# Performance work log

Measured on AMD Instinct MI355X. Metric: run time of the kernel, lower is better.

Reference implementation:

```python
import jax, jax.numpy as jnp
import numpy as np

B, IN_DIM, D, P = 256, 1024, 512, 2048


def setup_inputs() -> dict:
    key = jax.random.key(0)
    ks = jax.random.split(key, 7)
    return {
        "x": jax.random.normal(ks[0], (B, IN_DIM), dtype=jnp.float32),
        "y": jax.random.randint(ks[1], (B,), 0, P),
        "Wb": jax.random.normal(ks[2], (D, IN_DIM), dtype=jnp.float32) * 0.02,
        "bb": jax.random.normal(ks[3], (D,), dtype=jnp.float32) * 0.02,
        "Wm": jax.random.normal(ks[4], (P, D), dtype=jnp.float32) * 0.02,
        "bm": jax.random.normal(ks[5], (P,), dtype=jnp.float32) * 0.02,
        "proxies": jax.random.normal(ks[6], (P, D), dtype=jnp.float32),
    }


def reference(x, y, Wb, bb, Wm, bm, proxies):
    # backbone: Linear(in_dim -> D)
    feat = x @ Wb.T + bb                         # [B, D]
    # L2-norm regularizer: mean of per-row L2 norms
    reg_e = jnp.mean(jnp.sqrt(jnp.sum(feat * feat, axis=1)))
    # multi: classification head Linear(D -> P)
    out = feat @ Wm.T + bm                       # [B, P]
    # squared euclidean distance to each proxy (broadcast diff + square + sum)
    den = jnp.sum((feat[:, None, :] - proxies[None, :, :]) ** 2, axis=2)  # [B, P]
    # cross-entropy on negated distances
    logp = jax.nn.log_softmax(-den, axis=1)      # [B, P]
    loss = -jnp.mean(jnp.take_along_axis(logp, y[:, None], axis=1))
    return out, loss, reg_e
```

## Files before the change

kernel.cpp:

```cpp
#include <hip/hip_runtime.h>
#include <hip/hip_bf16.h>
#include <math.h>

#define NB   256
#define KIN  1024
#define ND   512
#define NP   2048
#define NTOT 4096

typedef __bf16 bf16x8 __attribute__((ext_vector_type(8)));
typedef float  f32x4  __attribute__((ext_vector_type(4)));
typedef unsigned short ush8 __attribute__((ext_vector_type(8)));

#define OFF_WPB    0u
#define OFF_FEAT32 4194304u
#define OFF_FEATB  4718592u
#define OFF_PN2    4980736u
#define OFF_LOGITS 4988928u

__device__ __forceinline__ ush8 pack8(float4 f0, float4 f1) {
    union { ush8 v; __hip_bfloat162 h[4]; } o;
    o.h[0] = __float22bfloat162_rn(make_float2(f0.x, f0.y));
    o.h[1] = __float22bfloat162_rn(make_float2(f0.z, f0.w));
    o.h[2] = __float22bfloat162_rn(make_float2(f1.x, f1.y));
    o.h[3] = __float22bfloat162_rn(make_float2(f1.z, f1.w));
    return o.v;
}
__device__ __forceinline__ unsigned short f2bf(float v) {
    union { __hip_bfloat16 h; unsigned short u; } c;
    c.h = __float2bfloat16(v);
    return c.u;
}

__global__ __launch_bounds__(256) void k_fa(
    const float* __restrict__ x, const float* __restrict__ Wb,
    const float* __restrict__ bb,
    const float* __restrict__ Wm, const float* __restrict__ prox,
    unsigned short* __restrict__ WPb, float* __restrict__ pn2,
    float* __restrict__ feat32, unsigned short* __restrict__ featb,
    float* __restrict__ tail)
{
    __shared__ unsigned short As[2][64 * 32];
    __shared__ unsigned short Bs[2][64 * 32];
    const int t = threadIdx.x, lane = t & 63, w = t >> 6;

    if (blockIdx.x >= 32) {
        const int pb = blockIdx.x - 32;
        if (pb == 0 && t < 2) tail[t] = 0.f;
#pragma unroll
        for (int i = 0; i < 4; ++i) {
            const int r = pb * 16 + w * 4 + i;
            const float* src = (r < NP) ? (Wm + (size_t)r * ND)
                                        : (prox + (size_t)(r - NP) * ND);
            float4 v0 = *(const float4*)(src + lane * 8);
            float4 v1 = *(const float4*)(src + lane * 8 + 4);
            if (r < NP) {
                *(ush8*)(WPb + (size_t)r * ND + lane * 8) = pack8(v0, v1);
            } else {
                float s = v0.x*v0.x + v0.y*v0.y + v0.z*v0.z + v0.w*v0.w
                        + v1.x*v1.x + v1.y*v1.y + v1.z*v1.z + v1.w*v1.w;
#pragma unroll
                for (int off = 32; off; off >>= 1) s += __shfl_down(s, off);
                if (lane == 0) pn2[r - NP] = s;
                float4 d0 = make_float4(v0.x + v0.x, v0.y + v0.y,
                                        v0.z + v0.z, v0.w + v0.w);
                float4 d1 = make_float4(v1.x + v1.x, v1.y + v1.y,
                                        v1.z + v1.z, v1.w + v1.w);
                *(ush8*)(WPb + (size_t)r * ND + lane * 8) = pack8(d0, d1);
            }
        }
        return;
    }

    const int m0 = (blockIdx.x >> 3) * 64, n0 = (blockIdx.x & 7) * 64;
    const int srow = t >> 2, sc = (t & 3) * 8;
    const float* gA = x  + (size_t)(m0 + srow) * KIN + sc;
    const float* gB = Wb + (size_t)(n0 + srow) * KIN + sc;
    float4 a0 = *(const float4*)gA, a1 = *(const float4*)(gA + 4);
    float4 b0 = *(const float4*)gB, b1 = *(const float4*)(gB + 4);
    f32x4 acc[2][2] = {};
    const int wm = (w >> 1) * 32, wn = (w & 1) * 32;
    const int fr = lane & 15, fcol = (lane >> 4) * 8;

    for (int ks = 0; ks < KIN / 32; ++ks) {
        *(ush8*)&As[ks & 1][srow * 32 + sc] = pack8(a0, a1);
        *(ush8*)&Bs[ks & 1][srow * 32 + sc] = pack8(b0, b1);
        __syncthreads();
        if (ks + 1 < KIN / 32) {
            a0 = *(const float4*)(gA + (ks + 1) * 32);
            a1 = *(const float4*)(gA + (ks + 1) * 32 + 4);
            b0 = *(const float4*)(gB + (ks + 1) * 32);
            b1 = *(const float4*)(gB + (ks + 1) * 32 + 4);
        }
        const unsigned short* as = &As[ks & 1][0];
        const unsigned short* bs = &Bs[ks & 1][0];
        bf16x8 af0 = *(const bf16x8*)&as[(wm      + fr) * 32 + fcol];
        bf16x8 af1 = *(const bf16x8*)&as[(wm + 16 + fr) * 32 + fcol];
        bf16x8 bf0 = *(const bf16x8*)&bs[(wn      + fr) * 32 + fcol];
        bf16x8 bf1 = *(const bf16x8*)&bs[(wn + 16 + fr) * 32 + fcol];
        acc[0][0] = __builtin_amdgcn_mfma_f32_16x16x32_bf16(af0, bf0, acc[0][0], 0, 0, 0);
        acc[0][1] = __builtin_amdgcn_mfma_f32_16x16x32_bf16(af0, bf1, acc[0][1], 0, 0, 0);
        acc[1][0] = __builtin_amdgcn_mfma_f32_16x16x32_bf16(af1, bf0, acc[1][0], 0, 0, 0);
        acc[1][1] = __builtin_amdgcn_mfma_f32_16x16x32_bf16(af1, bf1, acc[1][1], 0, 0, 0);
    }

    const int q = lane >> 4;
#pragma unroll
    for (int i = 0; i < 2; ++i)
#pragma unroll
        for (int j = 0; j < 2; ++j) {
            const int n = n0 + wn + 16 * j + fr;
            const float bbn = bb[n];
#pragma unroll
            for (int r = 0; r < 4; ++r) {
                const int m = m0 + wm + 16 * i + q * 4 + r;
                const float v = acc[i][j][r] + bbn;
                feat32[m * ND + n] = v;
                featb [m * ND + n] = f2bf(v);
            }
        }
}

__global__ __launch_bounds__(256) void k_fb(
    const unsigned short* __restrict__ featb,
    const unsigned short* __restrict__ WPb,
    const float* __restrict__ bm, const float* __restrict__ pn2,
    float* __restrict__ out, float* __restrict__ logits)
{
    __shared__ unsigned short As[2][64 * 32];
    __shared__ unsigned short Bs[2][64 * 32];
    const int t = threadIdx.x, lane = t & 63, w = t >> 6;
    const int n0 = blockIdx.x * 64;
    const int m0 = blockIdx.y * 64;
    const int srow = t >> 2, sc = (t & 3) * 8;
    const unsigned short* gA = featb + (size_t)(m0 + srow) * ND + sc;
    const unsigned short* gB = WPb   + (size_t)(n0 + srow) * ND + sc;
    ush8 va = *(const ush8*)gA;
    ush8 vb = *(const ush8*)gB;
    f32x4 acc[2][2] = {};
    const int wm = (w >> 1) * 32, wn = (w & 1) * 32;
    const int fr = lane & 15, fcol = (lane >> 4) * 8;

    for (int ks = 0; ks < ND / 32; ++ks) {
        *(ush8*)&As[ks & 1][srow * 32 + sc] = va;
        *(ush8*)&Bs[ks & 1][srow * 32 + sc] = vb;
        __syncthreads();
        if (ks + 1 < ND / 32) {
            va = *(const ush8*)(gA + (ks + 1) * 32);
            vb = *(const ush8*)(gB + (ks + 1) * 32);
        }
        const unsigned short* as = &As[ks & 1][0];
        const unsigned short* bs = &Bs[ks & 1][0];
        bf16x8 af0 = *(const bf16x8*)&as[(wm      + fr) * 32 + fcol];
        bf16x8 af1 = *(const bf16x8*)&as[(wm + 16 + fr) * 32 + fcol];
        bf16x8 bf0 = *(const bf16x8*)&bs[(wn      + fr) * 32 + fcol];
        bf16x8 bf1 = *(const bf16x8*)&bs[(wn + 16 + fr) * 32 + fcol];
        acc[0][0] = __builtin_amdgcn_mfma_f32_16x16x32_bf16(af0, bf0, acc[0][0], 0, 0, 0);
        acc[0][1] = __builtin_amdgcn_mfma_f32_16x16x32_bf16(af0, bf1, acc[0][1], 0, 0, 0);
        acc[1][0] = __builtin_amdgcn_mfma_f32_16x16x32_bf16(af1, bf0, acc[1][0], 0, 0, 0);
        acc[1][1] = __builtin_amdgcn_mfma_f32_16x16x32_bf16(af1, bf1, acc[1][1], 0, 0, 0);
    }

    const bool isProxy = (n0 >= NP);
    const int q = lane >> 4;
#pragma unroll
    for (int i = 0; i < 2; ++i)
#pragma unroll
        for (int j = 0; j < 2; ++j) {
            const int n = n0 + wn + 16 * j + fr;
            const float cadd = isProxy ? pn2[n - NP] : bm[n];
#pragma unroll
            for (int r = 0; r < 4; ++r) {
                const int m = m0 + wm + 16 * i + q * 4 + r;
                const float v = acc[i][j][r];
                if (isProxy) logits[m * NP + (n - NP)] = v - cadd;
                else         out[m * NP + n] = v + cadd;
            }
        }
}

__device__ __forceinline__ float block_reduce(float v, float* sred, int op)
{
    const int lane = threadIdx.x & 63, wave = threadIdx.x >> 6;
#pragma unroll
    for (int off = 32; off; off >>= 1) {
        float o = __shfl_down(v, off);
        v = op ? fmaxf(v, o) : (v + o);
    }
    if (lane == 0) sred[wave] = v;
    __syncthreads();
    if (threadIdx.x == 0) {
        float r = sred[0];
#pragma unroll
        for (int wv = 1; wv < 4; ++wv) r = op ? fmaxf(r, sred[wv]) : (r + sred[wv]);
        sred[0] = r;
    }
    __syncthreads();
    float r = sred[0];
    __syncthreads();
    return r;
}

__global__ __launch_bounds__(256) void k_fc(
    const float* __restrict__ feat32, const float* __restrict__ logits,
    const int* __restrict__ y, float* __restrict__ tail)
{
    __shared__ float sred[4];
    const int b = blockIdx.x, t = threadIdx.x;

    float v0 = feat32[b * ND + t];
    float v1 = feat32[b * ND + t + 256];
    float fn2 = block_reduce(v0 * v0 + v1 * v1, sred, 0);

    const float* lr = logits + (size_t)b * NP;
    float lv[8], mx = -INFINITY;
#pragma unroll
    for (int j = 0; j < 8; ++j) { lv[j] = lr[t + 256 * j]; mx = fmaxf(mx, lv[j]); }
    float MX = block_reduce(mx, sred, 1);
    float es = 0.f;
#pragma unroll
    for (int j = 0; j < 8; ++j) es += __expf(lv[j] - MX);
    float SUM = block_reduce(es, sred, 0);

    if (t == 0) {
        float ly = lr[y[b]];
        float lp = ly - MX - __logf(SUM);
        atomicAdd(&tail[0], -lp * (1.0f / (float)NB));
        atomicAdd(&tail[1], sqrtf(fn2) * (1.0f / (float)NB));
    }
}

extern "C" void kernel_launch(void* const* d_in, const int* in_sizes, int n_in,
                              void* d_out, int out_size, void* d_ws, size_t ws_size,
                              hipStream_t stream)
{
    const float* x       = (const float*)d_in[0];
    const int*   y       = (const int*)  d_in[1];
    const float* Wb      = (const float*)d_in[2];
    const float* bb      = (const float*)d_in[3];
    const float* Wm      = (const float*)d_in[4];
    const float* bm      = (const float*)d_in[5];
    const float* proxies = (const float*)d_in[6];

    char* ws = (char*)d_ws;
    unsigned short* WPb    = (unsigned short*)(ws + OFF_WPB);
    float*          feat32 = (float*)(ws + OFF_FEAT32);
    unsigned short* featb  = (unsigned short*)(ws + OFF_FEATB);
    float*          pn2    = (float*)(ws + OFF_PN2);
    float*          logits = (float*)(ws + OFF_LOGITS);

    float* out  = (float*)d_out;
    float* tail = out + (size_t)NB * NP;

    k_fa<<<dim3(288), dim3(256), 0, stream>>>(
        x, Wb, bb, Wm, proxies, WPb, pn2, feat32, featb, tail);
    k_fb<<<dim3(NTOT / 64, NB / 64), dim3(256), 0, stream>>>(
        featb, WPb, bm, pn2, out, logits);
    k_fc<<<dim3(NB), dim3(256), 0, stream>>>(feat32, logits, y, tail);
}
```

Before: 108.7 us.

## Drop LDS staging in both GEMMs; per-wave tiles loaded directly from global

Both GEMM kernels stop staging tiles through shared memory with barriers. Each wave now loads its MFMA fragments straight from global memory and owns an independent output tile: 32x32 in the backbone GEMM and 32x64 in the head/proxy GEMM, which gets 128 blocks instead of 256. This removes LDS writes, reads and __syncthreads. In exchange it loses data reuse across waves, so there is more global/L2 traffic and uncoalesced strided row loads, and the second GEMM runs fewer blocks.

```diff
diff --git a/kernel.cpp b/kernel.cpp
--- a/kernel.cpp
+++ b/kernel.cpp
@@ -31,6 +31,17 @@
     c.h = __float2bfloat16(v);
     return c.u;
 }
+__device__ __forceinline__ bf16x8 ldf8(const float* p) {
+    float4 v0 = *(const float4*)p, v1 = *(const float4*)(p + 4);
+    union { ush8 u; bf16x8 b; } c;
+    c.u = pack8(v0, v1);
+    return c.b;
+}
+__device__ __forceinline__ bf16x8 ldb8(const unsigned short* p) {
+    union { ush8 u; bf16x8 b; } c;
+    c.u = *(const ush8*)p;
+    return c.b;
+}
 
 __global__ __launch_bounds__(256) void k_fa(
     const float* __restrict__ x, const float* __restrict__ Wb,
@@ -40,8 +51,6 @@
     float* __restrict__ feat32, unsigned short* __restrict__ featb,
     float* __restrict__ tail)
 {
-    __shared__ unsigned short As[2][64 * 32];
-    __shared__ unsigned short Bs[2][64 * 32];
     const int t = threadIdx.x, lane = t & 63, w = t >> 6;
 
     if (blockIdx.x >= 32) {
@@ -72,32 +81,21 @@
         return;
     }
 
-    const int m0 = (blockIdx.x >> 3) * 64, n0 = (blockIdx.x & 7) * 64;
-    const int srow = t >> 2, sc = (t & 3) * 8;
-    const float* gA = x  + (size_t)(m0 + srow) * KIN + sc;
-    const float* gB = Wb + (size_t)(n0 + srow) * KIN + sc;
-    float4 a0 = *(const float4*)gA, a1 = *(const float4*)(gA + 4);
-    float4 b0 = *(const float4*)gB, b1 = *(const float4*)(gB + 4);
+    const int wid = blockIdx.x * 4 + w;
+    const int m0 = (wid >> 4) * 32, n0 = (wid & 15) * 32;
+    const int fr = lane & 15, ck = (lane >> 4) * 8;
+    const float* pA0 = x  + (size_t)(m0 + fr) * KIN + ck;
+    const float* pA1 = pA0 + 16 * KIN;
+    const float* pB0 = Wb + (size_t)(n0 + fr) * KIN + ck;
+    const float* pB1 = pB0 + 16 * KIN;
     f32x4 acc[2][2] = {};
-    const int wm = (w >> 1) * 32, wn = (w & 1) * 32;
-    const int fr = lane & 15, fcol = (lane >> 4) * 8;
-
+#pragma unroll 4
     for (int ks = 0; ks < KIN / 32; ++ks) {
-        *(ush8*)&As[ks & 1][srow * 32 + sc] = pack8(a0, a1);
-        *(ush8*)&Bs[ks & 1][srow * 32 + sc] = pack8(b0, b1);
-        __syncthreads();
-        if (ks + 1 < KIN / 32) {
-            a0 = *(const float4*)(gA + (ks + 1) * 32);
-            a1 = *(const float4*)(gA + (ks + 1) * 32 + 4);
-            b0 = *(const float4*)(gB + (ks + 1) * 32);
-            b1 = *(const float4*)(gB + (ks + 1) * 32 + 4);
-        }
-        const unsigned short* as = &As[ks & 1][0];
-        const unsigned short* bs = &Bs[ks & 1][0];
-        bf16x8 af0 = *(const bf16x8*)&as[(wm      + fr) * 32 + fcol];
-        bf16x8 af1 = *(const bf16x8*)&as[(wm + 16 + fr) * 32 + fcol];
-        bf16x8 bf0 = *(const bf16x8*)&bs[(wn      + fr) * 32 + fcol];
-        bf16x8 bf1 = *(const bf16x8*)&bs[(wn + 16 + fr) * 32 + fcol];
+        const int off = ks * 32;
+        bf16x8 af0 = ldf8(pA0 + off);
+        bf16x8 af1 = ldf8(pA1 + off);
+        bf16x8 bf0 = ldf8(pB0 + off);
+        bf16x8 bf1 = ldf8(pB1 + off);
         acc[0][0] = __builtin_amdgcn_mfma_f32_16x16x32_bf16(af0, bf0, acc[0][0], 0, 0, 0);
         acc[0][1] = __builtin_amdgcn_mfma_f32_16x16x32_bf16(af0, bf1, acc[0][1], 0, 0, 0);
         acc[1][0] = __builtin_amdgcn_mfma_f32_16x16x32_bf16(af1, bf0, acc[1][0], 0, 0, 0);
@@ -109,11 +107,11 @@
     for (int i = 0; i < 2; ++i)
 #pragma unroll
         for (int j = 0; j < 2; ++j) {
-            const int n = n0 + wn + 16 * j + fr;
+            const int n = n0 + 16 * j + fr;
             const float bbn = bb[n];
 #pragma unroll
             for (int r = 0; r < 4; ++r) {
-                const int m = m0 + wm + 16 * i + q * 4 + r;
+                const int m = m0 + 16 * i + q * 4 + r;
                 const float v = acc[i][j][r] + bbn;
                 feat32[m * ND + n] = v;
                 featb [m * ND + n] = f2bf(v);
@@ -127,56 +125,54 @@
     const float* __restrict__ bm, const float* __restrict__ pn2,
     float* __restrict__ out, float* __restrict__ logits)
 {
-    __shared__ unsigned short As[2][64 * 32];
-    __shared__ unsigned short Bs[2][64 * 32];
     const int t = threadIdx.x, lane = t & 63, w = t >> 6;
-    const int n0 = blockIdx.x * 64;
-    const int m0 = blockIdx.y * 64;
-    const int srow = t >> 2, sc = (t & 3) * 8;
-    const unsigned short* gA = featb + (size_t)(m0 + srow) * ND + sc;
-    const unsigned short* gB = WPb   + (size_t)(n0 + srow) * ND + sc;
-    ush8 va = *(const ush8*)gA;
-    ush8 vb = *(const ush8*)gB;
-    f32x4 acc[2][2] = {};
-    const int wm = (w >> 1) * 32, wn = (w & 1) * 32;
-    const int fr = lane & 15, fcol = (lane >> 4) * 8;
-
+    const int wid = blockIdx.x * 4 + w;
+    const int m0 = (wid >> 6) * 32, n0 = (wid & 63) * 64;
+    const int fr = lane & 15, ck = (lane >> 4) * 8;
+
+    const unsigned short* pA0 = featb + (size_t)(m0 + fr) * ND + ck;
+    const unsigned short* pA1 = pA0 + 16 * ND;
+    const unsigned short* pB0 = WPb + (size_t)(n0      + fr) * ND + ck;
+    const unsigned short* pB1 = WPb + (size_t)(n0 + 16 + fr) * ND + ck;
+    const unsigned short* pB2 = WPb + (size_t)(n0 + 32 + fr) * ND + ck;
+    const unsigned short* pB3 = WPb + (size_t)(n0 + 48 + fr) * ND + ck;
+
+    f32x4 acc[2][4] = {};
+#pragma unroll 4
     for (int ks = 0; ks < ND / 32; ++ks) {
-        *(ush8*)&As[ks & 1][srow * 32 + sc] = va;
-        *(ush8*)&Bs[ks & 1][srow * 32 + sc] = vb;
-        __syncthreads();
-        if (ks + 1 < ND / 32) {
-            va = *(const ush8*)(gA + (ks + 1) * 32);
-            vb = *(const ush8*)(gB + (ks + 1) * 32);
-        }
-        const unsigned short* as = &As[ks & 1][0];
-        const unsigned short* bs = &Bs[ks & 1][0];
-        bf16x8 af0 = *(const bf16x8*)&as[(wm      + fr) * 32 + fcol];
-        bf16x8 af1 = *(const bf16x8*)&as[(wm + 16 + fr) * 32 + fcol];
-        bf16x8 bf0 = *(const bf16x8*)&bs[(wn      + fr) * 32 + fcol];
-        bf16x8 bf1 = *(const bf16x8*)&bs[(wn + 16 + fr) * 32 + fcol];
+        const int off = ks * 32;
+        bf16x8 af0 = ldb8(pA0 + off);
+        bf16x8 af1 = ldb8(pA1 + off);
+        bf16x8 bf0 = ldb8(pB0 + off);
+        bf16x8 bf1 = ldb8(pB1 + off);
+        bf16x8 bf2 = ldb8(pB2 + off);
+        bf16x8 bf3 = ldb8(pB3 + off);
         acc[0][0] = __builtin_amdgcn_mfma_f32_16x16x32_bf16(af0, bf0, acc[0][0], 0, 0, 0);
         acc[0][1] = __builtin_amdgcn_mfma_f32_16x16x32_bf16(af0, bf1, acc[0][1], 0, 0, 0);
+        acc[0][2] = __builtin_amdgcn_mfma_f32_16x16x32_bf16(af0, bf2, acc[0][2], 0, 0, 0);
+        acc[0][3] = __builtin_amdgcn_mfma_f32_16x16x32_bf16(af0, bf3, acc[0][3], 0, 0, 0);
         acc[1][0] = __builtin_amdgcn_mfma_f32_16x16x32_bf16(af1, bf0, acc[1][0], 0, 0, 0);
         acc[1][1] = __builtin_amdgcn_mfma_f32_16x16x32_bf16(af1, bf1, acc[1][1], 0, 0, 0);
+        acc[1][2] = __builtin_amdgcn_mfma_f32_16x16x32_bf16(af1, bf2, acc[1][2], 0, 0, 0);
+        acc[1][3] = __builtin_amdgcn_mfma_f32_16x16x32_bf16(af1, bf3, acc[1][3], 0, 0, 0);
     }
 
     const bool isProxy = (n0 >= NP);
     const int q = lane >> 4;
 #pragma unroll
-    for (int i = 0; i < 2; ++i)
-#pragma unroll
-        for (int j = 0; j < 2; ++j) {
-            const int n = n0 + wn + 16 * j + fr;
-            const float cadd = isProxy ? pn2[n - NP] : bm[n];
+    for (int j = 0; j < 4; ++j) {
+        const int n = n0 + 16 * j + fr;
+        const float cadd = isProxy ? pn2[n - NP] : bm[n];
+#pragma unroll
+        for (int i = 0; i < 2; ++i)
 #pragma unroll
             for (int r = 0; r < 4; ++r) {
-                const int m = m0 + wm + 16 * i + q * 4 + r;
+                const int m = m0 + 16 * i + q * 4 + r;
                 const float v = acc[i][j][r];
                 if (isProxy) logits[m * NP + (n - NP)] = v - cadd;
                 else         out[m * NP + n] = v + cadd;
             }
-        }
+    }
 }
 
 __device__ __forceinline__ float block_reduce(float v, float* sred, int op)
@@ -254,7 +250,7 @@
 
     k_fa<<<dim3(288), dim3(256), 0, stream>>>(
         x, Wb, bb, Wm, proxies, WPb, pn2, feat32, featb, tail);
-    k_fb<<<dim3(NTOT / 64, NB / 64), dim3(256), 0, stream>>>(
+    k_fb<<<dim3(128), dim3(256), 0, stream>>>(
         featb, WPb, bm, pn2, out, logits);
     k_fc<<<dim3(NB), dim3(256), 0, stream>>>(feat32, logits, y, tail);
 }
```

Measured after the change: 131.1 us. +20.6%, slower.

## Fuse three kernels into one cooperative kernel with grid syncs and split-K backbone GEMM

Applied to the files above, without the earlier changes.

Merges the backbone GEMM, the head/proxy GEMM, and the softmax/regularizer reduction into a single cooperative launch of 256 blocks, separated by grid-wide syncs. This removes two kernel launch gaps. The backbone GEMM now uses 128 blocks of 32x32 tiles with split-K across the four waves, loading operands straight from global memory and reducing through shared memory. The remaining 128 blocks pack the weights. The cost is grid.sync overhead, and the main GEMM now runs on only 256 blocks (256 of 4096/64*4 tiles) instead of 256 independent launches' worth of scheduling.

```diff
diff --git a/kernel.cpp b/kernel.cpp
--- a/kernel.cpp
+++ b/kernel.cpp
@@ -1,6 +1,9 @@
 #include <hip/hip_runtime.h>
+#include <hip/hip_cooperative_groups.h>
 #include <hip/hip_bf16.h>
 #include <math.h>
+
+namespace cg = cooperative_groups;
 
 #define NB   256
 #define KIN  1024
@@ -31,25 +34,55 @@
     c.h = __float2bfloat16(v);
     return c.u;
 }
-
-__global__ __launch_bounds__(256) void k_fa(
-    const float* __restrict__ x, const float* __restrict__ Wb,
-    const float* __restrict__ bb,
-    const float* __restrict__ Wm, const float* __restrict__ prox,
+__device__ __forceinline__ bf16x8 ldf8(const float* p) {
+    float4 v0 = *(const float4*)p, v1 = *(const float4*)(p + 4);
+    union { ush8 u; bf16x8 b; } c;
+    c.u = pack8(v0, v1);
+    return c.b;
+}
+
+__device__ __forceinline__ float block_reduce(float v, float* sred, int op)
+{
+    const int lane = threadIdx.x & 63, wave = threadIdx.x >> 6;
+#pragma unroll
+    for (int off = 32; off; off >>= 1) {
+        float o = __shfl_down(v, off);
+        v = op ? fmaxf(v, o) : (v + o);
+    }
+    if (lane == 0) sred[wave] = v;
+    __syncthreads();
+    if (threadIdx.x == 0) {
+        float r = sred[0];
+#pragma unroll
+        for (int wv = 1; wv < 4; ++wv) r = op ? fmaxf(r, sred[wv]) : (r + sred[wv]);
+        sred[0] = r;
+    }
+    __syncthreads();
+    float r = sred[0];
+    __syncthreads();
+    return r;
+}
+
+__global__ __launch_bounds__(256) void k_all(
+    const float* __restrict__ x, const int* __restrict__ y,
+    const float* __restrict__ Wb, const float* __restrict__ bb,
+    const float* __restrict__ Wm, const float* __restrict__ bm,
+    const float* __restrict__ prox,
     unsigned short* __restrict__ WPb, float* __restrict__ pn2,
     float* __restrict__ feat32, unsigned short* __restrict__ featb,
+    float* __restrict__ logits, float* __restrict__ out,
     float* __restrict__ tail)
 {
-    __shared__ unsigned short As[2][64 * 32];
-    __shared__ unsigned short Bs[2][64 * 32];
+    cg::grid_group grid = cg::this_grid();
     const int t = threadIdx.x, lane = t & 63, w = t >> 6;
-
-    if (blockIdx.x >= 32) {
-        const int pb = blockIdx.x - 32;
+    __shared__ __align__(16) float smemf[4 * 1056];
+
+    if (blockIdx.x >= 128) {
+        const int pb = blockIdx.x - 128;
         if (pb == 0 && t < 2) tail[t] = 0.f;
 #pragma unroll
-        for (int i = 0; i < 4; ++i) {
-            const int r = pb * 16 + w * 4 + i;
+        for (int i = 0; i < 8; ++i) {
+            const int r = pb * 32 + w * 8 + i;
             const float* src = (r < NP) ? (Wm + (size_t)r * ND)
                                         : (prox + (size_t)(r - NP) * ND);
             float4 v0 = *(const float4*)(src + lane * 8);
@@ -69,164 +102,131 @@
                 *(ush8*)(WPb + (size_t)r * ND + lane * 8) = pack8(d0, d1);
             }
         }
-        return;
-    }
-
-    const int m0 = (blockIdx.x >> 3) * 64, n0 = (blockIdx.x & 7) * 64;
-    const int srow = t >> 2, sc = (t & 3) * 8;
-    const float* gA = x  + (size_t)(m0 + srow) * KIN + sc;
-    const float* gB = Wb + (size_t)(n0 + srow) * KIN + sc;
-    float4 a0 = *(const float4*)gA, a1 = *(const float4*)(gA + 4);
-    float4 b0 = *(const float4*)gB, b1 = *(const float4*)(gB + 4);
-    f32x4 acc[2][2] = {};
-    const int wm = (w >> 1) * 32, wn = (w & 1) * 32;
-    const int fr = lane & 15, fcol = (lane >> 4) * 8;
-
-    for (int ks = 0; ks < KIN / 32; ++ks) {
-        *(ush8*)&As[ks & 1][srow * 32 + sc] = pack8(a0, a1);
-        *(ush8*)&Bs[ks & 1][srow * 32 + sc] = pack8(b0, b1);
+    } else {
+        const int m0 = (blockIdx.x >> 4) * 32, n0 = (blockIdx.x & 15) * 32;
+        const int fr = lane & 15, ck = (lane >> 4) * 8;
+        const float* pA0 = x  + (size_t)(m0 + fr) * KIN + w * 256 + ck;
+        const float* pA1 = pA0 + 16 * KIN;
+        const float* pB0 = Wb + (size_t)(n0 + fr) * KIN + w * 256 + ck;
+        const float* pB1 = pB0 + 16 * KIN;
+        f32x4 acc[2][2] = {};
+#pragma unroll
+        for (int ks = 0; ks < 8; ++ks) {
+            const int off = ks * 32;
+            bf16x8 af0 = ldf8(pA0 + off);
+            bf16x8 af1 = ldf8(pA1 + off);
+            bf16x8 bf0 = ldf8(pB0 + off);
+            bf16x8 bf1 = ldf8(pB1 + off);
+            acc[0][0] = __builtin_amdgcn_mfma_f32_16x16x32_bf16(af0, bf0, acc[0][0], 0, 0, 0);
+            acc[0][1] = __builtin_amdgcn_mfma_f32_16x16x32_bf16(af0, bf1, acc[0][1], 0, 0, 0);
+            acc[1][0] = __builtin_amdgcn_mfma_f32_16x16x32_bf16(af1, bf0, acc[1][0], 0, 0, 0);
+            acc[1][1] = __builtin_amdgcn_mfma_f32_16x16x32_bf16(af1, bf1, acc[1][1], 0, 0, 0);
+        }
+        float* red = smemf + w * 1056;
+        const int q = lane >> 4;
+#pragma unroll
+        for (int i = 0; i < 2; ++i)
+#pragma unroll
+            for (int j = 0; j < 2; ++j)
+#pragma unroll
+                for (int r = 0; r < 4; ++r)
+                    red[(16 * i + q * 4 + r) * 33 + 16 * j + fr] = acc[i][j][r];
         __syncthreads();
-        if (ks + 1 < KIN / 32) {
-            a0 = *(const float4*)(gA + (ks + 1) * 32);
-            a1 = *(const float4*)(gA + (ks + 1) * 32 + 4);
-            b0 = *(const float4*)(gB + (ks + 1) * 32);
-            b1 = *(const float4*)(gB + (ks + 1) * 32 + 4);
-        }
-        const unsigned short* as = &As[ks & 1][0];
-        const unsigned short* bs = &Bs[ks & 1][0];
-        bf16x8 af0 = *(const bf16x8*)&as[(wm      + fr) * 32 + fcol];
-        bf16x8 af1 = *(const bf16x8*)&as[(wm + 16 + fr) * 32 + fcol];
-        bf16x8 bf0 = *(const bf16x8*)&bs[(wn      + fr) * 32 + fcol];
-        bf16x8 bf1 = *(const bf16x8*)&bs[(wn + 16 + fr) * 32 + fcol];
-        acc[0][0] = __builtin_amdgcn_mfma_f32_16x16x32_bf16(af0, bf0, acc[0][0], 0, 0, 0);
-        acc[0][1] = __builtin_amdgcn_mfma_f32_16x16x32_bf16(af0, bf1, acc[0][1], 0, 0, 0);
-        acc[1][0] = __builtin_amdgcn_mfma_f32_16x16x32_bf16(af1, bf0, acc[1][0], 0, 0, 0);
-        acc[1][1] = __builtin_amdgcn_mfma_f32_16x16x32_bf16(af1, bf1, acc[1][1], 0, 0, 0);
-    }
-
-    const int q = lane >> 4;
-#pragma unroll
-    for (int i = 0; i < 2; ++i)
-#pragma unroll
-        for (int j = 0; j < 2; ++j) {
-            const int n = n0 + wn + 16 * j + fr;
-            const float bbn = bb[n];
-#pragma unroll
-            for (int r = 0; r < 4; ++r) {
-                const int m = m0 + wm + 16 * i + q * 4 + r;
-                const float v = acc[i][j][r] + bbn;
-                feat32[m * ND + n] = v;
-                featb [m * ND + n] = f2bf(v);
+#pragma unroll
+        for (int e = t; e < 1024; e += 256) {
+            const int row = e >> 5, col = e & 31;
+            const int idx = row * 33 + col;
+            float v = smemf[idx] + smemf[idx + 1056]
+                    + smemf[idx + 2112] + smemf[idx + 3168];
+            const int n = n0 + col;
+            const float val = v + bb[n];
+            feat32[(m0 + row) * ND + n] = val;
+            featb [(m0 + row) * ND + n] = f2bf(val);
+        }
+    }
+
+    __threadfence();
+    grid.sync();
+
+    {
+        unsigned short* As = (unsigned short*)smemf;
+        unsigned short* Bs = As + 4096;
+        const int n0 = (blockIdx.x & 63) * 64;
+        const int m0 = (blockIdx.x >> 6) * 64;
+        const int srow = t >> 2, sc = (t & 3) * 8;
+        const unsigned short* gA = featb + (size_t)(m0 + srow) * ND + sc;
+        const unsigned short* gB = WPb   + (size_t)(n0 + srow) * ND + sc;
+        ush8 va = *(const ush8*)gA;
+        ush8 vb = *(const ush8*)gB;
+        f32x4 acc[2][2] = {};
+        const int wm = (w >> 1) * 32, wn = (w & 1) * 32;
+        const int fr = lane & 15, fcol = (lane >> 4) * 8;
+
+        for (int ks = 0; ks < ND / 32; ++ks) {
+            *(ush8*)&As[(ks & 1) * 2048 + srow * 32 + sc] = va;
+            *(ush8*)&Bs[(ks & 1) * 2048 + srow * 32 + sc] = vb;
+            __syncthreads();
+            if (ks + 1 < ND / 32) {
+                va = *(const ush8*)(gA + (ks + 1) * 32);
+                vb = *(const ush8*)(gB + (ks + 1) * 32);
             }
-        }
-}
-
-__global__ __launch_bounds__(256) void k_fb(
-    const unsigned short* __restrict__ featb,
-    const unsigned short* __restrict__ WPb,
-    const float* __restrict__ bm, const float* __restrict__ pn2,
-    float* __restrict__ out, float* __restrict__ logits)
-{
-    __shared__ unsigned short As[2][64 * 32];
-    __shared__ unsigned short Bs[2][64 * 32];
-    const int t = threadIdx.x, lane = t & 63, w = t >> 6;
-    const int n0 = blockIdx.x * 64;
-    const int m0 = blockIdx.y * 64;
-    const int srow = t >> 2, sc = (t & 3) * 8;
-    const unsigned short* gA = featb + (size_t)(m0 + srow) * ND + sc;
-    const unsigned short* gB = WPb   + (size_t)(n0 + srow) * ND + sc;
-    ush8 va = *(const ush8*)gA;
-    ush8 vb = *(const ush8*)gB;
-    f32x4 acc[2][2] = {};
-    const int wm = (w >> 1) * 32, wn = (w & 1) * 32;
-    const int fr = lane & 15, fcol = (lane >> 4) * 8;
-
-    for (int ks = 0; ks < ND / 32; ++ks) {
-        *(ush8*)&As[ks & 1][srow * 32 + sc] = va;
-        *(ush8*)&Bs[ks & 1][srow * 32 + sc] = vb;
-        __syncthreads();
-        if (ks + 1 < ND / 32) {
-            va = *(const ush8*)(gA + (ks + 1) * 32);
-            vb = *(const ush8*)(gB + (ks + 1) * 32);
-        }
-        const unsigned short* as = &As[ks & 1][0];
-        const unsigned short* bs = &Bs[ks & 1][0];
-        bf16x8 af0 = *(const bf16x8*)&as[(wm      + fr) * 32 + fcol];
-        bf16x8 af1 = *(const bf16x8*)&as[(wm + 16 + fr) * 32 + fcol];
-        bf16x8 bf0 = *(const bf16x8*)&bs[(wn      + fr) * 32 + fcol];
-        bf16x8 bf1 = *(const bf16x8*)&bs[(wn + 16 + fr) * 32 + fcol];
-        acc[0][0] = __builtin_amdgcn_mfma_f32_16x16x32_bf16(af0, bf0, acc[0][0], 0, 0, 0);
-        acc[0][1] = __builtin_amdgcn_mfma_f32_16x16x32_bf16(af0, bf1, acc[0][1], 0, 0, 0);
-        acc[1][0] = __builtin_amdgcn_mfma_f32_16x16x32_bf16(af1, bf0, acc[1][0], 0, 0, 0);
-        acc[1][1] = __builtin_amdgcn_mfma_f32_16x16x32_bf16(af1, bf1, acc[1][1], 0, 0, 0);
-    }
-
-    const bool isProxy = (n0 >= NP);
-    const int q = lane >> 4;
-#pragma unroll
-    for (int i = 0; i < 2; ++i)
-#pragma unroll
-        for (int j = 0; j < 2; ++j) {
-            const int n = n0 + wn + 16 * j + fr;
-            const float cadd = isProxy ? pn2[n - NP] : bm[n];
-#pragma unroll
-            for (int r = 0; r < 4; ++r) {
-                const int m = m0 + wm + 16 * i + q * 4 + r;
-                const float v = acc[i][j][r];
-                if (isProxy) logits[m * NP + (n - NP)] = v - cadd;
-                else         out[m * NP + n] = v + cadd;
+            const unsigned short* as = &As[(ks & 1) * 2048];
+            const unsigned short* bs = &Bs[(ks & 1) * 2048];
+            bf16x8 af0 = *(const bf16x8*)&as[(wm      + fr) * 32 + fcol];
+            bf16x8 af1 = *(const bf16x8*)&as[(wm + 16 + fr) * 32 + fcol];
+            bf16x8 bf0 = *(const bf16x8*)&bs[(wn      + fr) * 32 + fcol];
+            bf16x8 bf1 = *(const bf16x8*)&bs[(wn + 16 + fr) * 32 + fcol];
+            acc[0][0] = __builtin_amdgcn_mfma_f32_16x16x32_bf16(af0, bf0, acc[0][0], 0, 0, 0);
+            acc[0][1] = __builtin_amdgcn_mfma_f32_16x16x32_bf16(af0, bf1, acc[0][1], 0, 0, 0);
+            acc[1][0] = __builtin_amdgcn_mfma_f32_16x16x32_bf16(af1, bf0, acc[1][0], 0, 0, 0);
+            acc[1][1] = __builtin_amdgcn_mfma_f32_16x16x32_bf16(af1, bf1, acc[1][1], 0, 0, 0);
+        }
+
+        const bool isProxy = (n0 >= NP);
+        const int q = lane >> 4;
+#pragma unroll
+        for (int i = 0; i < 2; ++i)
+#pragma unroll
+            for (int j = 0; j < 2; ++j) {
+                const int n = n0 + wn + 16 * j + fr;
+                const float cadd = isProxy ? pn2[n - NP] : bm[n];
+#pragma unroll
+                for (int r = 0; r < 4; ++r) {
+                    const int m = m0 + wm + 16 * i + q * 4 + r;
+                    const float v = acc[i][j][r];
+                    if (isProxy) logits[m * NP + (n - NP)] = v - cadd;
+                    else         out[m * NP + n] = v + cadd;
+                }
             }
-        }
-}
-
-__device__ __forceinline__ float block_reduce(float v, float* sred, int op)
-{
-    const int lane = threadIdx.x & 63, wave = threadIdx.x >> 6;
-#pragma unroll
-    for (int off = 32; off; off >>= 1) {
-        float o = __shfl_down(v, off);
-        v = op ? fmaxf(v, o) : (v + o);
-    }
-    if (lane == 0) sred[wave] = v;
-    __syncthreads();
-    if (threadIdx.x == 0) {
-        float r = sred[0];
-#pragma unroll
-        for (int wv = 1; wv < 4; ++wv) r = op ? fmaxf(r, sred[wv]) : (r + sred[wv]);
-        sred[0] = r;
-    }
-    __syncthreads();
-    float r = sred[0];
-    __syncthreads();
-    return r;
-}
-
-__global__ __launch_bounds__(256) void k_fc(
-    const float* __restrict__ feat32, const float* __restrict__ logits,
-    const int* __restrict__ y, float* __restrict__ tail)
-{
-    __shared__ float sred[4];
-    const int b = blockIdx.x, t = threadIdx.x;
-
-    float v0 = feat32[b * ND + t];
-    float v1 = feat32[b * ND + t + 256];
-    float fn2 = block_reduce(v0 * v0 + v1 * v1, sred, 0);
-
-    const float* lr = logits + (size_t)b * NP;
-    float lv[8], mx = -INFINITY;
-#pragma unroll
-    for (int j = 0; j < 8; ++j) { lv[j] = lr[t + 256 * j]; mx = fmaxf(mx, lv[j]); }
-    float MX = block_reduce(mx, sred, 1);
-    float es = 0.f;
-#pragma unroll
-    for (int j = 0; j < 8; ++j) es += __expf(lv[j] - MX);
-    float SUM = block_reduce(es, sred, 0);
-
-    if (t == 0) {
-        float ly = lr[y[b]];
-        float lp = ly - MX - __logf(SUM);
-        atomicAdd(&tail[0], -lp * (1.0f / (float)NB));
-        atomicAdd(&tail[1], sqrtf(fn2) * (1.0f / (float)NB));
+    }
+
+    __threadfence();
+    grid.sync();
+
+    {
+        float* sred = smemf;
+        const int b = blockIdx.x;
+
+        float v0 = feat32[b * ND + t];
+        float v1 = feat32[b * ND + t + 256];
+        float fn2 = block_reduce(v0 * v0 + v1 * v1, sred, 0);
+
+        const float* lr = logits + (size_t)b * NP;
+        float lv[8], mx = -INFINITY;
+#pragma unroll
+        for (int j = 0; j < 8; ++j) { lv[j] = lr[t + 256 * j]; mx = fmaxf(mx, lv[j]); }
+        float MX = block_reduce(mx, sred, 1);
+        float es = 0.f;
+#pragma unroll
+        for (int j = 0; j < 8; ++j) es += __expf(lv[j] - MX);
+        float SUM = block_reduce(es, sred, 0);
+
+        if (t == 0) {
+            float ly = lr[y[b]];
+            float lp = ly - MX - __logf(SUM);
+            atomicAdd(&tail[0], -lp * (1.0f / (float)NB));
+            atomicAdd(&tail[1], sqrtf(fn2) * (1.0f / (float)NB));
+        }
     }
 }
 
@@ -252,9 +252,10 @@
     float* out  = (float*)d_out;
     float* tail = out + (size_t)NB * NP;
 
-    k_fa<<<dim3(288), dim3(256), 0, stream>>>(
-        x, Wb, bb, Wm, proxies, WPb, pn2, feat32, featb, tail);
-    k_fb<<<dim3(NTOT / 64, NB / 64), dim3(256), 0, stream>>>(
-        featb, WPb, bm, pn2, out, logits);
-    k_fc<<<dim3(NB), dim3(256), 0, stream>>>(feat32, logits, y, tail);
-}
+    void* args[] = { (void*)&x, (void*)&y, (void*)&Wb, (void*)&bb,
+                     (void*)&Wm, (void*)&bm, (void*)&proxies,
+                     (void*)&WPb, (void*)&pn2, (void*)&feat32, (void*)&featb,
+                     (void*)&logits, (void*)&out, (void*)&tail };
+    hipLaunchCooperativeKernel((void*)k_all, dim3(256), dim3(256),
+                               args, 0, stream);
+}
```

New measurement: 234.0 us. +115.4%, slower.
